# Performance work log

Hardware: AMD Instinct MI355X
Metric: run time of the kernel (lower is better)

## Reference

```python
import jax, jax.numpy as jnp
import numpy as np

TEMPERATURE = 8.0      # sqrt(d_head=64), matches init temperature
MASK_FILL = -1e32      # masked_softmax memory_efficient fill value
B, L, D = 16, 2048, 64


def setup_inputs() -> dict:
    key = jax.random.key(0)
    kq, kk, kv, kd, km = jax.random.split(key, 5)
    q = jax.random.normal(kq, (B, L, D), dtype=jnp.float32)
    k = jax.random.normal(kk, (B, L, D), dtype=jnp.float32)
    v = jax.random.normal(kv, (B, L, D), dtype=jnp.float32)
    diag_mask = jax.random.randint(kd, (B, L, L), 0, 2, dtype=jnp.int32)  # 1=keep, 0=mask
    mask = jax.random.randint(km, (B, L, L), 0, 2, dtype=jnp.int32).astype(jnp.bool_)  # True=mask out
    return {"q": q, "k": k, "v": v, "diag_mask": diag_mask, "mask": mask}


def reference(q, k, v, diag_mask, mask):
    # attn = q @ k^T / temperature   -> [B, Lq, Lk]
    attn = jnp.einsum('bqd,bkd->bqk', q, k) / TEMPERATURE
    # attn.masked_fill(mask, -inf)
    attn = jnp.where(mask, -jnp.inf, attn)
    # masked_softmax(attn, diag_mask, memory_efficient=True):
    #   masked_fill((1 - diag_mask).bool(), -1e32) then softmax
    attn = jnp.where(diag_mask == 0, MASK_FILL, attn)
    attn = jax.nn.softmax(attn, axis=-1)
    # output = attn @ v
    output = jnp.einsum('bqk,bkd->bqd', attn, v)
    return output, attn
```

## Files before the change

### kernel.cpp

```cpp
#include <hip/hip_runtime.h>
#include <math.h>

#define NB 16
#define SL 2048
#define HD 64
#define TQ 16
#define BK 64
#define NT (SL / BK)
#define SCALE 0.125f
#define TSTR 72

typedef _Float16 half8 __attribute__((ext_vector_type(8)));
typedef float floatx4 __attribute__((ext_vector_type(4)));

__device__ __forceinline__ half8 load_frag_f32(const float* p) {
  floatx4 f0 = *(const floatx4*)p;
  floatx4 f1 = *(const floatx4*)(p + 4);
  half8 h;
  h[0] = (_Float16)f0[0]; h[1] = (_Float16)f0[1];
  h[2] = (_Float16)f0[2]; h[3] = (_Float16)f0[3];
  h[4] = (_Float16)f1[0]; h[5] = (_Float16)f1[1];
  h[6] = (_Float16)f1[2]; h[7] = (_Float16)f1[3];
  return h;
}

__global__ __launch_bounds__(256) void attn_kernel(
    const float* __restrict__ Q, const float* __restrict__ K,
    const float* __restrict__ V, const int* __restrict__ DM,
    const int* __restrict__ MMk, float* __restrict__ Out,
    float* __restrict__ Attn)
{
  const int qt   = blockIdx.x;
  const int b    = blockIdx.y;
  const int tid  = (int)threadIdx.x;
  const int w    = tid >> 6;
  const int lane = tid & 63;
  const int quad = lane >> 4;
  const int nl   = lane & 15;

  const int qbase    = qt * TQ;
  const size_t bLD   = (size_t)b * SL * HD;
  const size_t mbase = ((size_t)b * SL + qbase) * SL;

  __shared__ __align__(16) _Float16 tileP[2][TQ * TSTR];
  __shared__ float redbuf[4][TQ];

  half8 aq0, aq1;
  {
    const float* qp = Q + bLD + (size_t)(qbase + nl) * HD + quad * 8;
    aq0 = load_frag_f32(qp);
    aq1 = load_frag_f32(qp + 32);
  }

  float esum[4] = {0.f, 0.f, 0.f, 0.f};
  unsigned kbits[4] = {0u, 0u, 0u, 0u};

  #pragma unroll 2
  for (int kt = 0; kt < NT; ++kt) {
    const float* kp = K + bLD + (size_t)(kt * BK + w * 16 + nl) * HD + quad * 8;
    half8 bk0 = load_frag_f32(kp);
    half8 bk1 = load_frag_f32(kp + 32);
    floatx4 acc = {0.f, 0.f, 0.f, 0.f};
    acc = __builtin_amdgcn_mfma_f32_16x16x32_f16(aq0, bk0, acc, 0, 0, 0);
    acc = __builtin_amdgcn_mfma_f32_16x16x32_f16(aq1, bk1, acc, 0, 0, 0);
    const int col = kt * BK + w * 16 + nl;
    int dm[4], mk[4];
    #pragma unroll
    for (int r = 0; r < 4; ++r) {
      const size_t ma = mbase + (size_t)(quad * 4 + r) * SL + col;
      dm[r] = __builtin_nontemporal_load(DM + ma);
      mk[r] = __builtin_nontemporal_load(MMk + ma);
    }
    #pragma unroll
    for (int r = 0; r < 4; ++r) {
      const unsigned keep = (dm[r] != 0) && (mk[r] == 0);
      kbits[r] |= keep << kt;
      const float e = keep ? __expf(acc[r] * SCALE) : 0.f;
      esum[r] += e;
    }
  }

  #pragma unroll
  for (int r = 0; r < 4; ++r) {
    float s = esum[r];
    #pragma unroll
    for (int off = 1; off < 16; off <<= 1)
      s = s + __shfl_xor(s, off, 64);
    esum[r] = s;
  }
  if (nl == 0) {
    #pragma unroll
    for (int r = 0; r < 4; ++r)
      redbuf[w][quad * 4 + r] = esum[r];
  }
  __syncthreads();

  float is[4];
  #pragma unroll
  for (int r = 0; r < 4; ++r) {
    const int row = quad * 4 + r;
    const float t = redbuf[0][row] + redbuf[1][row] + redbuf[2][row] + redbuf[3][row];
    is[r] = (t > 0.f) ? 1.f / t : 0.f;
  }

  floatx4 oacc = {0.f, 0.f, 0.f, 0.f};
  for (int kt = 0; kt < NT; ++kt) {
    const float* kp = K + bLD + (size_t)(kt * BK + w * 16 + nl) * HD + quad * 8;
    half8 bk0 = load_frag_f32(kp);
    half8 bk1 = load_frag_f32(kp + 32);
    floatx4 acc = {0.f, 0.f, 0.f, 0.f};
    acc = __builtin_amdgcn_mfma_f32_16x16x32_f16(aq0, bk0, acc, 0, 0, 0);
    acc = __builtin_amdgcn_mfma_f32_16x16x32_f16(aq1, bk1, acc, 0, 0, 0);

    _Float16* tp = tileP[kt & 1];
    const int col = kt * BK + w * 16 + nl;
    #pragma unroll
    for (int r = 0; r < 4; ++r) {
      const unsigned keep = (kbits[r] >> kt) & 1u;
      const float e = keep ? __expf(acc[r] * SCALE) : 0.f;
      tp[(quad * 4 + r) * TSTR + w * 16 + nl] = (_Float16)e;
      __builtin_nontemporal_store(e * is[r],
          Attn + mbase + (size_t)(quad * 4 + r) * SL + col);
    }
    half8 bv0, bv1;
    const float* vp = V + bLD + (size_t)(kt * BK + quad * 8) * HD + w * 16 + nl;
    #pragma unroll
    for (int j = 0; j < 8; ++j) {
      bv0[j] = (_Float16)vp[(size_t)j * HD];
      bv1[j] = (_Float16)vp[(size_t)(j + 32) * HD];
    }
    __syncthreads();

    half8 ap0 = *(const half8*)(tp + nl * TSTR + quad * 8);
    half8 ap1 = *(const half8*)(tp + nl * TSTR + quad * 8 + 32);
    oacc = __builtin_amdgcn_mfma_f32_16x16x32_f16(ap0, bv0, oacc, 0, 0, 0);
    oacc = __builtin_amdgcn_mfma_f32_16x16x32_f16(ap1, bv1, oacc, 0, 0, 0);
  }

  {
    float* op = Out + ((size_t)b * SL + qbase) * HD;
    #pragma unroll
    for (int r = 0; r < 4; ++r)
      op[(size_t)(quad * 4 + r) * HD + w * 16 + nl] = oacc[r] * is[r];
  }
}

extern "C" void kernel_launch(void* const* d_in, const int* in_sizes, int n_in,
                              void* d_out, int out_size, void* d_ws, size_t ws_size,
                              hipStream_t stream) {
  const float* Q  = (const float*)d_in[0];
  const float* K  = (const float*)d_in[1];
  const float* V  = (const float*)d_in[2];
  const int* DM   = (const int*)d_in[3];
  const int* MMk  = (const int*)d_in[4];
  float* Out  = (float*)d_out;
  float* Attn = (float*)d_out + (size_t)NB * SL * HD;
  dim3 grid(SL / TQ, NB);
  attn_kernel<<<grid, 256, 0, stream>>>(Q, K, V, DM, MMk, Out, Attn);
}
```

Before: 858.4 us.

## Cache unnormalized scores in LDS and split keys across 16 waves

The kernel now runs 1024 threads per block, with 16 waves splitting the key dimension into four segments. Each wave computes exp scores once and stores them in fp16 in a full-row shared-memory buffer, so the second QK^T pass and the recomputed exps go away. The attention output is written from shared memory as coalesced vector stores, and the PV partial sums from the four segments are reduced through shared memory. The trade-off is a large LDS footprint (about 66KB), which limits occupancy, and the written attention probabilities now come from fp16-rounded exps, which lowers their precision.

```diff
diff --git a/kernel.cpp b/kernel.cpp
--- a/kernel.cpp
+++ b/kernel.cpp
@@ -8,9 +8,10 @@
 #define BK 64
 #define NT (SL / BK)
 #define SCALE 0.125f
-#define TSTR 72
+#define SSTRIDE 2056
 
 typedef _Float16 half8 __attribute__((ext_vector_type(8)));
+typedef _Float16 half4 __attribute__((ext_vector_type(4)));
 typedef float floatx4 __attribute__((ext_vector_type(4)));
 
 __device__ __forceinline__ half8 load_frag_f32(const float* p) {
@@ -24,7 +25,7 @@
   return h;
 }
 
-__global__ __launch_bounds__(256) void attn_kernel(
+__global__ __launch_bounds__(1024) void attn_kernel(
     const float* __restrict__ Q, const float* __restrict__ K,
     const float* __restrict__ V, const int* __restrict__ DM,
     const int* __restrict__ MMk, float* __restrict__ Out,
@@ -34,6 +35,8 @@
   const int b    = blockIdx.y;
   const int tid  = (int)threadIdx.x;
   const int w    = tid >> 6;
+  const int w4   = w & 3;
+  const int seg  = w >> 2;
   const int lane = tid & 63;
   const int quad = lane >> 4;
   const int nl   = lane & 15;
@@ -42,8 +45,10 @@
   const size_t bLD   = (size_t)b * SL * HD;
   const size_t mbase = ((size_t)b * SL + qbase) * SL;
 
-  __shared__ __align__(16) _Float16 tileP[2][TQ * TSTR];
-  __shared__ float redbuf[4][TQ];
+  __shared__ __align__(16) _Float16 S[TQ * SSTRIDE];
+  __shared__ float redbuf[16][16];
+  __shared__ float sinv_s[TQ];
+  __shared__ float obuf[3][TQ][68];
 
   half8 aq0, aq1;
   {
@@ -52,31 +57,33 @@
     aq1 = load_frag_f32(qp + 32);
   }
 
+  const int colbase = w4 * 16 + nl;
   float esum[4] = {0.f, 0.f, 0.f, 0.f};
-  unsigned kbits[4] = {0u, 0u, 0u, 0u};
 
   #pragma unroll 2
-  for (int kt = 0; kt < NT; ++kt) {
-    const float* kp = K + bLD + (size_t)(kt * BK + w * 16 + nl) * HD + quad * 8;
+  for (int i = 0; i < 8; ++i) {
+    const int kt  = seg * 8 + i;
+    const int col = kt * BK + colbase;
+    int dm[4], mk[4];
+    const int* dmp = DM  + mbase + col;
+    const int* mkp = MMk + mbase + col;
+    #pragma unroll
+    for (int r = 0; r < 4; ++r) {
+      dm[r] = __builtin_nontemporal_load(dmp + (size_t)(quad * 4 + r) * SL);
+      mk[r] = __builtin_nontemporal_load(mkp + (size_t)(quad * 4 + r) * SL);
+    }
+    const float* kp = K + bLD + (size_t)(kt * BK + colbase) * HD + quad * 8;
     half8 bk0 = load_frag_f32(kp);
     half8 bk1 = load_frag_f32(kp + 32);
     floatx4 acc = {0.f, 0.f, 0.f, 0.f};
     acc = __builtin_amdgcn_mfma_f32_16x16x32_f16(aq0, bk0, acc, 0, 0, 0);
     acc = __builtin_amdgcn_mfma_f32_16x16x32_f16(aq1, bk1, acc, 0, 0, 0);
-    const int col = kt * BK + w * 16 + nl;
-    int dm[4], mk[4];
     #pragma unroll
     for (int r = 0; r < 4; ++r) {
-      const size_t ma = mbase + (size_t)(quad * 4 + r) * SL + col;
-      dm[r] = __builtin_nontemporal_load(DM + ma);
-      mk[r] = __builtin_nontemporal_load(MMk + ma);
-    }
-    #pragma unroll
-    for (int r = 0; r < 4; ++r) {
-      const unsigned keep = (dm[r] != 0) && (mk[r] == 0);
-      kbits[r] |= keep << kt;
+      const bool keep = (dm[r] != 0) && (mk[r] == 0);
       const float e = keep ? __expf(acc[r] * SCALE) : 0.f;
       esum[r] += e;
+      S[(quad * 4 + r) * SSTRIDE + col] = (_Float16)e;
     }
   }
 
@@ -85,7 +92,7 @@
     float s = esum[r];
     #pragma unroll
     for (int off = 1; off < 16; off <<= 1)
-      s = s + __shfl_xor(s, off, 64);
+      s += __shfl_xor(s, off, 64);
     esum[r] = s;
   }
   if (nl == 0) {
@@ -94,54 +101,61 @@
       redbuf[w][quad * 4 + r] = esum[r];
   }
   __syncthreads();
+  if (tid < TQ) {
+    float t = 0.f;
+    #pragma unroll
+    for (int j = 0; j < 16; ++j) t += redbuf[j][tid];
+    sinv_s[tid] = (t > 0.f) ? 1.f / t : 0.f;
+  }
+  __syncthreads();
 
-  float is[4];
-  #pragma unroll
-  for (int r = 0; r < 4; ++r) {
-    const int row = quad * 4 + r;
-    const float t = redbuf[0][row] + redbuf[1][row] + redbuf[2][row] + redbuf[3][row];
-    is[r] = (t > 0.f) ? 1.f / t : 0.f;
+  {
+    const float is = sinv_s[w];
+    const _Float16* srow = &S[w * SSTRIDE];
+    float* arow = Attn + mbase + (size_t)w * SL;
+    #pragma unroll 4
+    for (int it = 0; it < 8; ++it) {
+      const int c = it * 256 + lane * 4;
+      half4 e4 = *(const half4*)(srow + c);
+      floatx4 o;
+      #pragma unroll
+      for (int j = 0; j < 4; ++j) o[j] = (float)e4[j] * is;
+      __builtin_nontemporal_store(o, (floatx4*)(arow + c));
+    }
   }
 
   floatx4 oacc = {0.f, 0.f, 0.f, 0.f};
-  for (int kt = 0; kt < NT; ++kt) {
-    const float* kp = K + bLD + (size_t)(kt * BK + w * 16 + nl) * HD + quad * 8;
-    half8 bk0 = load_frag_f32(kp);
-    half8 bk1 = load_frag_f32(kp + 32);
-    floatx4 acc = {0.f, 0.f, 0.f, 0.f};
-    acc = __builtin_amdgcn_mfma_f32_16x16x32_f16(aq0, bk0, acc, 0, 0, 0);
-    acc = __builtin_amdgcn_mfma_f32_16x16x32_f16(aq1, bk1, acc, 0, 0, 0);
-
-    _Float16* tp = tileP[kt & 1];
-    const int col = kt * BK + w * 16 + nl;
-    #pragma unroll
-    for (int r = 0; r < 4; ++r) {
-      const unsigned keep = (kbits[r] >> kt) & 1u;
-      const float e = keep ? __expf(acc[r] * SCALE) : 0.f;
-      tp[(quad * 4 + r) * TSTR + w * 16 + nl] = (_Float16)e;
-      __builtin_nontemporal_store(e * is[r],
-          Attn + mbase + (size_t)(quad * 4 + r) * SL + col);
-    }
+  #pragma unroll 2
+  for (int i = 0; i < 8; ++i) {
+    const int kt = seg * 8 + i;
+    half8 ap0 = *(const half8*)(&S[nl * SSTRIDE + kt * BK + quad * 8]);
+    half8 ap1 = *(const half8*)(&S[nl * SSTRIDE + kt * BK + quad * 8 + 32]);
     half8 bv0, bv1;
-    const float* vp = V + bLD + (size_t)(kt * BK + quad * 8) * HD + w * 16 + nl;
+    const float* vp = V + bLD + (size_t)(kt * BK + quad * 8) * HD + colbase;
     #pragma unroll
     for (int j = 0; j < 8; ++j) {
       bv0[j] = (_Float16)vp[(size_t)j * HD];
       bv1[j] = (_Float16)vp[(size_t)(j + 32) * HD];
     }
-    __syncthreads();
-
-    half8 ap0 = *(const half8*)(tp + nl * TSTR + quad * 8);
-    half8 ap1 = *(const half8*)(tp + nl * TSTR + quad * 8 + 32);
     oacc = __builtin_amdgcn_mfma_f32_16x16x32_f16(ap0, bv0, oacc, 0, 0, 0);
     oacc = __builtin_amdgcn_mfma_f32_16x16x32_f16(ap1, bv1, oacc, 0, 0, 0);
   }
 
-  {
+  if (seg != 0) {
+    #pragma unroll
+    for (int r = 0; r < 4; ++r)
+      obuf[seg - 1][quad * 4 + r][colbase] = oacc[r];
+  }
+  __syncthreads();
+  if (seg == 0) {
     float* op = Out + ((size_t)b * SL + qbase) * HD;
     #pragma unroll
-    for (int r = 0; r < 4; ++r)
-      op[(size_t)(quad * 4 + r) * HD + w * 16 + nl] = oacc[r] * is[r];
+    for (int r = 0; r < 4; ++r) {
+      const int row = quad * 4 + r;
+      const float v = oacc[r] + obuf[0][row][colbase] +
+                      obuf[1][row][colbase] + obuf[2][row][colbase];
+      op[(size_t)row * HD + colbase] = v * sinv_s[row];
+    }
   }
 }
 
@@ -156,5 +170,5 @@
   float* Out  = (float*)d_out;
   float* Attn = (float*)d_out + (size_t)NB * SL * HD;
   dim3 grid(SL / TQ, NB);
-  attn_kernel<<<grid, 256, 0, stream>>>(Q, K, V, DM, MMk, Out, Attn);
+  attn_kernel<<<grid, 1024, 0, stream>>>(Q, K, V, DM, MMk, Out, Attn);
 }
```

Measured after the change: 772.4 us. 1.11x faster.
